# Kernel optimization log

Measured on AMD Instinct MI355X. Metric: run time of the kernel, lower is better.

## Reference

```python
import jax, jax.numpy as jnp
import numpy as np

B, S, U, H = 4, 2048, 1024, 8
HD = U // H
EPS = 1e-8


def setup_inputs() -> dict:
    key = jax.random.key(0)
    ks = jax.random.split(key, 10)
    sc = 1.0 / np.sqrt(U)
    x = jax.random.normal(ks[0], (B, S, U), dtype=jnp.float32)
    Wq = jax.random.normal(ks[1], (U, U), dtype=jnp.float32) * sc
    bq = jnp.zeros((U,), dtype=jnp.float32)
    Wk = jax.random.normal(ks[2], (U, U), dtype=jnp.float32) * sc
    bk = jnp.zeros((U,), dtype=jnp.float32)
    Wv = jax.random.normal(ks[3], (U, U), dtype=jnp.float32) * sc
    bv = jnp.zeros((U,), dtype=jnp.float32)
    Wr = jax.random.normal(ks[4], (U, U), dtype=jnp.float32) * sc
    br = jnp.zeros((U,), dtype=jnp.float32)
    gamma = jnp.ones((U,), dtype=jnp.float32)
    beta = jnp.zeros((U,), dtype=jnp.float32)
    return {"x": x, "Wq": Wq, "bq": bq, "Wk": Wk, "bk": bk, "Wv": Wv,
            "bv": bv, "Wr": Wr, "br": br, "gamma": gamma, "beta": beta}


def reference(x, Wq, bq, Wk, bk, Wv, bv, Wr, br, gamma, beta):
    relu = jax.nn.relu
    q = relu(jnp.einsum('bsu,uv->bsv', x, Wq) + bq)
    k = relu(jnp.einsum('bsu,uv->bsv', x, Wk) + bk)
    v = relu(jnp.einsum('bsu,uv->bsv', x, Wv) + bv)
    res = relu(jnp.einsum('bsu,uv->bsv', x, Wr) + br)
    # Faithful to the original: a raw reshape (NOT split+transpose head split).
    q = q.reshape(B * H, S, HD)
    k = k.reshape(B * H, S, HD)
    v = v.reshape(B * H, S, HD)
    scores = jnp.einsum('nqd,nkd->nqk', q, k) / jnp.sqrt(jnp.float32(HD))
    weights = jax.nn.softmax(scores, axis=-1)
    # dropout_rate = 0.0 -> identity
    attn = jnp.einsum('nqk,nkd->nqd', weights, v)
    attn = attn.reshape(B, S, U)
    out = relu(attn + res)
    # custom LayerNorm (biased variance, eps inside sqrt)
    mean = jnp.mean(out, axis=-1, keepdims=True)
    var = jnp.mean(jnp.square(out - mean), axis=-1, keepdims=True)
    normed = (out - mean) / jnp.sqrt(var + EPS)
    return gamma * normed + beta
```

## Files before the change

kernel.cpp:

```cpp
#include <hip/hip_runtime.h>

typedef _Float16 half8_t __attribute__((ext_vector_type(8)));
typedef _Float16 half4_t __attribute__((ext_vector_type(4)));
typedef float floatx4 __attribute__((ext_vector_type(4)));

#define S_LEN 2048
#define U_DIM 1024
#define HD 128
#define M_TOT 8192
#define NHEADS 32


__device__ __forceinline__ void stage16(void* lds_base, const void* g_lane, int lane) {
#if defined(__has_builtin) && __has_builtin(__builtin_amdgcn_global_load_lds)
    __builtin_amdgcn_global_load_lds(
        (const __attribute__((address_space(1))) unsigned int*)g_lane,
        (__attribute__((address_space(3))) unsigned int*)lds_base, 16, 0, 0);
#else
    *(float4*)((char*)lds_base + lane * 16) = *(const float4*)g_lane;
#endif
}

__device__ __forceinline__ int swz(int row) { return (row >> 1) & 3; }

__global__ __launch_bounds__(256) void k_convert_x(const float* __restrict__ x,
                                                   _Float16* __restrict__ xh) {
    size_t i = (size_t)blockIdx.x * 256 + threadIdx.x;
    float4 v = ((const float4*)x)[i];
    half4_t h;
    h[0] = (_Float16)v.x; h[1] = (_Float16)v.y;
    h[2] = (_Float16)v.z; h[3] = (_Float16)v.w;
    ((half4_t*)xh)[i] = h;
}

__global__ __launch_bounds__(256) void k_transpose_w(const float* __restrict__ Wq,
                                                     const float* __restrict__ Wk,
                                                     const float* __restrict__ Wv,
                                                     const float* __restrict__ Wr,
                                                     _Float16* __restrict__ wt) {
    const int z = blockIdx.z;
    const float* W = (z == 0) ? Wq : (z == 1) ? Wk : (z == 2) ? Wv : Wr;
    _Float16* o = wt + (size_t)z * U_DIM * U_DIM;
    __shared__ float t[64][65];
    const int n0 = blockIdx.x * 64, k0 = blockIdx.y * 64;
    const int tid = threadIdx.x;
    for (int c = tid; c < 1024; c += 256) {
        int kk = c >> 4, nn = (c & 15) * 4;
        float4 v = *(const float4*)&W[(size_t)(k0 + kk) * U_DIM + n0 + nn];
        t[kk][nn] = v.x; t[kk][nn + 1] = v.y; t[kk][nn + 2] = v.z; t[kk][nn + 3] = v.w;
    }
    __syncthreads();
    for (int c = tid; c < 512; c += 256) {
        int nn = c >> 3, ks = (c & 7) * 8;
        half8_t h;
        for (int i = 0; i < 8; i++) h[i] = (_Float16)t[ks + i][nn];
        *(half8_t*)&o[(size_t)(n0 + nn) * U_DIM + k0 + ks] = h;
    }
}

__global__ __launch_bounds__(256) void k_qkvr_gemm(const _Float16* __restrict__ xh,
                                                   const _Float16* __restrict__ wt,
                                                   const float* __restrict__ bq,
                                                   const float* __restrict__ bk,
                                                   const float* __restrict__ bv,
                                                   const float* __restrict__ br,
                                                   _Float16* __restrict__ qh,
                                                   _Float16* __restrict__ kh,
                                                   _Float16* __restrict__ vh,
                                                   _Float16* __restrict__ resh) {
    const int b = blockIdx.x;
    const int xcd = b & 7, s = b >> 3;
    const int pair = xcd + 8 * (s & 3);
    const int m0 = (s >> 2) * 128;
    const int n0 = (pair & 7) * 128;
    const int z = pair >> 3;
    const _Float16* wz = wt + (size_t)z * U_DIM * U_DIM;

    __shared__ __align__(16) char AsB[8192];
    __shared__ __align__(16) char BsB[8192];
    __shared__ __align__(16) _Float16 Cs[128][136];

    const int tid = threadIdx.x;
    const int wave = tid >> 6, lane = tid & 63;
    const int lrow = lane & 15, quad = lane >> 4;
    const int wm = (wave >> 1) * 64, wn = (wave & 1) * 64;
    const int lr4 = lane >> 2;
    const int sseg = ((lane & 3) ^ swz(lr4)) * 16;

    floatx4 acc[4][4];
    for (int i = 0; i < 4; i++)
        for (int j = 0; j < 4; j++) acc[i][j] = (floatx4)0.0f;

    const char* xb = (const char*)xh;
    const char* wb = (const char*)wz;
    const int rsw = (quad ^ swz(lrow)) * 16;

    for (int k0 = 0; k0 < U_DIM; k0 += 32) {
        for (int t = 0; t < 2; t++) {
            int c = wave * 2 + t;
            stage16(AsB + c * 1024,
                    xb + (size_t)(m0 + c * 16 + lr4) * 2048 + k0 * 2 + sseg, lane);
            stage16(BsB + c * 1024,
                    wb + (size_t)(n0 + c * 16 + lr4) * 2048 + k0 * 2 + sseg, lane);
        }
        __syncthreads();
        half8_t af[4], bf[4];
        for (int i = 0; i < 4; i++)
            af[i] = *(const half8_t*)(AsB + ((wave >> 1) * 4 + i) * 1024 + lrow * 64 + rsw);
        for (int j = 0; j < 4; j++)
            bf[j] = *(const half8_t*)(BsB + ((wave & 1) * 4 + j) * 1024 + lrow * 64 + rsw);
        for (int i = 0; i < 4; i++)
            for (int j = 0; j < 4; j++)
                acc[i][j] = __builtin_amdgcn_mfma_f32_16x16x32_f16(af[i], bf[j], acc[i][j], 0, 0, 0);
        __syncthreads();
    }

    const float* bias = (z == 0) ? bq : (z == 1) ? bk : (z == 2) ? bv : br;
    _Float16* dst = (z == 0) ? qh : (z == 1) ? kh : (z == 2) ? vh : resh;

    for (int i = 0; i < 4; i++) {
        for (int j = 0; j < 4; j++) {
            int col = wn + j * 16 + lrow;
            float bcol = bias[n0 + col];
            for (int r = 0; r < 4; r++) {
                float v = acc[i][j][r] + bcol;
                Cs[wm + i * 16 + quad * 4 + r][col] = (_Float16)(v > 0.f ? v : 0.f);
            }
        }
    }
    __syncthreads();
    for (int c = tid; c < 2048; c += 256) {
        int row = c >> 4, seg = (c & 15) * 8;
        *(half8_t*)&dst[(size_t)(m0 + row) * U_DIM + n0 + seg] = *(half8_t*)&Cs[row][seg];
    }
}

__global__ __launch_bounds__(256) void k_transpose_v(const _Float16* __restrict__ vh,
                                                     _Float16* __restrict__ vt) {
    const int n = blockIdx.z;
    const int s0 = blockIdx.x * 64, d0 = blockIdx.y * 64;
    const _Float16* V = vh + (size_t)n * S_LEN * HD;
    _Float16* O = vt + (size_t)n * HD * S_LEN;
    __shared__ _Float16 t[64][72];
    const int tid = threadIdx.x;
    for (int c = tid; c < 512; c += 256) {
        int srow = c >> 3, off = (c & 7) * 8;
        *(half8_t*)&t[srow][off] = *(const half8_t*)&V[(size_t)(s0 + srow) * HD + d0 + off];
    }
    __syncthreads();
    for (int c = tid; c < 512; c += 256) {
        int drow = c >> 3, soff = (c & 7) * 8;
        half8_t h;
        for (int i = 0; i < 8; i++) h[i] = t[soff + i][drow];
        *(half8_t*)&O[(size_t)(d0 + drow) * S_LEN + s0 + soff] = h;
    }
}

__global__ __launch_bounds__(256, 2) void k_flash(const _Float16* __restrict__ qh,
                                                  const _Float16* __restrict__ kh,
                                                  const _Float16* __restrict__ vt,
                                                  float* __restrict__ Opart,
                                                  float* __restrict__ lpart) {
    const int head = blockIdx.x + 8 * (blockIdx.y & 3);
    const int m0 = (int)(blockIdx.y >> 2) * 128;
    const int kv2 = blockIdx.z;
    const _Float16* Q = qh + (size_t)head * S_LEN * HD;
    const char* Kb = (const char*)(kh + (size_t)head * S_LEN * HD);
    const char* Vb = (const char*)(vt + (size_t)head * HD * S_LEN);

    __shared__ __align__(16) char smem[51200];
    _Float16* Ps = (_Float16*)(smem + 32768);

    const int tid = threadIdx.x;
    const int w = tid >> 6, lane = tid & 63;
    const int lrow = lane & 15, quad = lane >> 4;
    const int lr4 = lane >> 2;
    const int sseg = ((lane & 3) ^ swz(lr4)) * 16;
    const int rsw = (quad ^ swz(lrow)) * 16;

    half8_t qf[2][4];
    for (int i = 0; i < 2; i++)
        for (int k0 = 0; k0 < 4; k0++)
            qf[i][k0] = *(const half8_t*)&Q[(size_t)(m0 + w * 32 + i * 16 + lrow) * HD + k0 * 32 + quad * 8];

    floatx4 acc_o[2][8];
    for (int i = 0; i < 2; i++)
        for (int j = 0; j < 8; j++) acc_o[i][j] = (floatx4)0.0f;
    float lp[2] = {0.0f, 0.0f};

    const float C1 = 0.12751742f;
    const int kt_end = kv2 * 16 + 16;

    for (int kt = kv2 * 16; kt < kt_end; ++kt) {
        if (kt != kv2 * 16) __syncthreads();
        for (int t = 0; t < 4; t++) {
            int c = w * 4 + t;
            int k0 = c >> 2, j = c & 3;
            stage16(smem + c * 1024,
                    Kb + (size_t)(kt * 64 + j * 16 + lr4) * 256 + k0 * 64 + sseg, lane);
        }
        for (int t = 0; t < 4; t++) {
            int c = w * 4 + t;
            int k0s = c >> 3, dg = c & 7;
            stage16(smem + 16384 + c * 1024,
                    Vb + (size_t)(dg * 16 + lr4) * 4096 + kt * 128 + k0s * 64 + sseg, lane);
        }
        __syncthreads();

        floatx4 acc_t[2][4];
        for (int i = 0; i < 2; i++)
            for (int j = 0; j < 4; j++) acc_t[i][j] = (floatx4)0.0f;
        for (int k0 = 0; k0 < 4; k0++)
            for (int j = 0; j < 4; j++) {
                half8_t kf = *(const half8_t*)(smem + (k0 * 4 + j) * 1024 + lrow * 64 + rsw);
                for (int i = 0; i < 2; i++)
                    acc_t[i][j] = __builtin_amdgcn_mfma_f32_16x16x32_f16(kf, qf[i][k0], acc_t[i][j], 0, 0, 0);
            }

        for (int i = 0; i < 2; i++)
            for (int j = 0; j < 4; j++) {
                floatx4 sv = acc_t[i][j] * C1 - 6.0f;
                half4_t ph;
                float p0 = exp2f(sv[0]), p1 = exp2f(sv[1]);
                float p2 = exp2f(sv[2]), p3 = exp2f(sv[3]);
                ph[0] = (_Float16)p0; ph[1] = (_Float16)p1;
                ph[2] = (_Float16)p2; ph[3] = (_Float16)p3;
                lp[i] += (p0 + p1) + (p2 + p3);
                *(half4_t*)&Ps[(w * 32 + i * 16 + lrow) * 72 + j * 16 + quad * 4] = ph;
            }

        for (int k0s = 0; k0s < 2; k0s++) {
            half8_t af[2];
            for (int i = 0; i < 2; i++)
                af[i] = *(const half8_t*)&Ps[(w * 32 + i * 16 + lrow) * 72 + k0s * 32 + quad * 8];
            for (int j = 0; j < 8; j++) {
                half8_t bv = *(const half8_t*)(smem + 16384 + (k0s * 8 + j) * 1024 + lrow * 64 + rsw);
                for (int i = 0; i < 2; i++)
                    acc_o[i][j] = __builtin_amdgcn_mfma_f32_16x16x32_f16(af[i], bv, acc_o[i][j], 0, 0, 0);
            }
        }
    }

    for (int i = 0; i < 2; i++) {
        lp[i] += __shfl_xor(lp[i], 16, 64);
        lp[i] += __shfl_xor(lp[i], 32, 64);
    }

    float* Od = Opart + (size_t)kv2 * ((size_t)NHEADS * S_LEN * HD) +
                ((size_t)head * S_LEN + m0) * HD;
    for (int i = 0; i < 2; i++)
        for (int j = 0; j < 8; j++)
            for (int r = 0; r < 4; r++)
                Od[(size_t)(w * 32 + i * 16 + quad * 4 + r) * HD + j * 16 + lrow] = acc_o[i][j][r];
    float* Ld = lpart + (size_t)kv2 * (NHEADS * S_LEN) + head * S_LEN + m0;
    if (quad == 0) {
        Ld[w * 32 + lrow] = lp[0];
        Ld[w * 32 + 16 + lrow] = lp[1];
    }
}

__global__ __launch_bounds__(256) void k_ln(const float* __restrict__ Opart,
                                            const float* __restrict__ lpart,
                                            const _Float16* __restrict__ resh,
                                            const float* __restrict__ gamma,
                                            const float* __restrict__ beta,
                                            float* __restrict__ out) {
    const int row = blockIdx.x;
    const int tid = threadIdx.x;
    const size_t e = (size_t)row * U_DIM + tid * 4;
    const size_t OH = (size_t)M_TOT * U_DIM;
    const int lidx = row * 8 + (tid >> 5);

    float4 a4 = *(const float4*)&Opart[e];
    float4 b4 = *(const float4*)&Opart[OH + e];
    float l = lpart[lidx] + lpart[NHEADS * S_LEN + lidx];
    float inv = 1.0f / l;
    half4_t rv = ((const half4_t*)(resh))[e >> 2];
    float4 gv = ((const float4*)gamma)[tid];
    float4 bv = ((const float4*)beta)[tid];

    float o[4];
    o[0] = fmaxf((a4.x + b4.x) * inv + (float)rv[0], 0.f);
    o[1] = fmaxf((a4.y + b4.y) * inv + (float)rv[1], 0.f);
    o[2] = fmaxf((a4.z + b4.z) * inv + (float)rv[2], 0.f);
    o[3] = fmaxf((a4.w + b4.w) * inv + (float)rv[3], 0.f);

    float s1 = (o[0] + o[1]) + (o[2] + o[3]);
    float s2 = (o[0] * o[0] + o[1] * o[1]) + (o[2] * o[2] + o[3] * o[3]);
    for (int off = 32; off; off >>= 1) {
        s1 += __shfl_xor(s1, off, 64);
        s2 += __shfl_xor(s2, off, 64);
    }
    __shared__ float red[8];
    const int wv = tid >> 6;
    if ((tid & 63) == 0) { red[wv] = s1; red[4 + wv] = s2; }
    __syncthreads();
    float ts1 = red[0] + red[1] + red[2] + red[3];
    float ts2 = red[4] + red[5] + red[6] + red[7];
    float mean = ts1 * (1.0f / 1024.0f);
    float var = ts2 * (1.0f / 1024.0f) - mean * mean;
    float rstd = rsqrtf(var + 1e-8f);
    float4 ov;
    ov.x = gv.x * (o[0] - mean) * rstd + bv.x;
    ov.y = gv.y * (o[1] - mean) * rstd + bv.y;
    ov.z = gv.z * (o[2] - mean) * rstd + bv.z;
    ov.w = gv.w * (o[3] - mean) * rstd + bv.w;
    ((float4*)(out))[e >> 2] = ov;
}

extern "C" void kernel_launch(void* const* d_in, const int* in_sizes, int n_in,
                              void* d_out, int out_size, void* d_ws, size_t ws_size,
                              hipStream_t stream) {
    const float* x     = (const float*)d_in[0];
    const float* Wq    = (const float*)d_in[1];
    const float* bq    = (const float*)d_in[2];
    const float* Wk    = (const float*)d_in[3];
    const float* bk    = (const float*)d_in[4];
    const float* Wv    = (const float*)d_in[5];
    const float* bv    = (const float*)d_in[6];
    const float* Wr    = (const float*)d_in[7];
    const float* br    = (const float*)d_in[8];
    const float* gamma = (const float*)d_in[9];
    const float* beta  = (const float*)d_in[10];
    float* out = (float*)d_out;

    char* p = (char*)d_ws;
    _Float16* xh = (_Float16*)p;    p += (size_t)M_TOT * U_DIM * 2;
    _Float16* wt = (_Float16*)p;    p += (size_t)4 * U_DIM * U_DIM * 2;
    _Float16* qh = (_Float16*)p;    p += (size_t)M_TOT * U_DIM * 2;
    _Float16* kh = (_Float16*)p;    p += (size_t)M_TOT * U_DIM * 2;
    _Float16* vh = (_Float16*)p;    p += (size_t)M_TOT * U_DIM * 2;
    _Float16* vt = (_Float16*)p;    p += (size_t)M_TOT * U_DIM * 2;
    _Float16* resh = (_Float16*)p;  p += (size_t)M_TOT * U_DIM * 2;
    float* Opart = (float*)p;       p += (size_t)2 * M_TOT * U_DIM * 4;
    float* lpart = (float*)p;

    k_convert_x<<<8192, 256, 0, stream>>>(x, xh);
    k_transpose_w<<<dim3(16, 16, 4), 256, 0, stream>>>(Wq, Wk, Wv, Wr, wt);
    k_qkvr_gemm<<<2048, 256, 0, stream>>>(xh, wt, bq, bk, bv, br, qh, kh, vh, resh);
    k_transpose_v<<<dim3(32, 2, 32), 256, 0, stream>>>(vh, vt);
    k_flash<<<dim3(8, 64, 2), 256, 0, stream>>>(qh, kh, vt, Opart, lpart);
    k_ln<<<8192, 256, 0, stream>>>(Opart, lpart, resh, gamma, beta, out);
}
```

Baseline: 307.0 us.

## Prefetch next tiles into registers, replacing direct global-to-LDS loads

In both the projection GEMM and the attention kernel, the direct global_load_lds staging is replaced by register prefetching. The next K-tile is loaded into registers while the current tile is being computed, then written to LDS at the top of the next iteration. The __syncthreads barriers become a custom s_waitcnt lgkmcnt(0) plus s_barrier, so vector-memory prefetches are not waited on at each barrier. This aims to hide global load latency behind MFMA work, at the cost of more registers (possible occupancy loss) and an extra barrier per attention iteration.

```diff
diff --git a/kernel.cpp b/kernel.cpp
--- a/kernel.cpp
+++ b/kernel.cpp
@@ -11,14 +11,8 @@
 #define NHEADS 32
 
 
-__device__ __forceinline__ void stage16(void* lds_base, const void* g_lane, int lane) {
-#if defined(__has_builtin) && __has_builtin(__builtin_amdgcn_global_load_lds)
-    __builtin_amdgcn_global_load_lds(
-        (const __attribute__((address_space(1))) unsigned int*)g_lane,
-        (__attribute__((address_space(3))) unsigned int*)lds_base, 16, 0, 0);
-#else
-    *(float4*)((char*)lds_base + lane * 16) = *(const float4*)g_lane;
-#endif
+__device__ __forceinline__ void barrier_lgkm() {
+    __asm__ volatile("s_waitcnt lgkmcnt(0)\ns_barrier" ::: "memory");
 }
 
 __device__ __forceinline__ int swz(int row) { return (row >> 1) & 3; }
@@ -86,24 +80,33 @@
     const int wm = (wave >> 1) * 64, wn = (wave & 1) * 64;
     const int lr4 = lane >> 2;
     const int sseg = ((lane & 3) ^ swz(lr4)) * 16;
+    const int rsw = (quad ^ swz(lrow)) * 16;
 
     floatx4 acc[4][4];
     for (int i = 0; i < 4; i++)
         for (int j = 0; j < 4; j++) acc[i][j] = (floatx4)0.0f;
 
-    const char* xb = (const char*)xh;
-    const char* wb = (const char*)wz;
-    const int rsw = (quad ^ swz(lrow)) * 16;
+    const char* xsrc = (const char*)xh + (size_t)(m0 + wave * 32 + lr4) * 2048 + sseg;
+    const char* wsrc = (const char*)wz + (size_t)(n0 + wave * 32 + lr4) * 2048 + sseg;
+
+    float4 areg[2], breg[2];
+    for (int t = 0; t < 2; t++) {
+        areg[t] = *(const float4*)(xsrc + t * 16 * 2048);
+        breg[t] = *(const float4*)(wsrc + t * 16 * 2048);
+    }
 
     for (int k0 = 0; k0 < U_DIM; k0 += 32) {
         for (int t = 0; t < 2; t++) {
-            int c = wave * 2 + t;
-            stage16(AsB + c * 1024,
-                    xb + (size_t)(m0 + c * 16 + lr4) * 2048 + k0 * 2 + sseg, lane);
-            stage16(BsB + c * 1024,
-                    wb + (size_t)(n0 + c * 16 + lr4) * 2048 + k0 * 2 + sseg, lane);
-        }
-        __syncthreads();
+            *(float4*)(AsB + (wave * 2 + t) * 1024 + lane * 16) = areg[t];
+            *(float4*)(BsB + (wave * 2 + t) * 1024 + lane * 16) = breg[t];
+        }
+        barrier_lgkm();
+        if (k0 + 32 < U_DIM) {
+            for (int t = 0; t < 2; t++) {
+                areg[t] = *(const float4*)(xsrc + t * 16 * 2048 + (k0 + 32) * 2);
+                breg[t] = *(const float4*)(wsrc + t * 16 * 2048 + (k0 + 32) * 2);
+            }
+        }
         half8_t af[4], bf[4];
         for (int i = 0; i < 4; i++)
             af[i] = *(const half8_t*)(AsB + ((wave >> 1) * 4 + i) * 1024 + lrow * 64 + rsw);
@@ -112,7 +115,7 @@
         for (int i = 0; i < 4; i++)
             for (int j = 0; j < 4; j++)
                 acc[i][j] = __builtin_amdgcn_mfma_f32_16x16x32_f16(af[i], bf[j], acc[i][j], 0, 0, 0);
-        __syncthreads();
+        barrier_lgkm();
     }
 
     const float* bias = (z == 0) ? bq : (z == 1) ? bk : (z == 2) ? bv : br;
@@ -189,23 +192,34 @@
     float lp[2] = {0.0f, 0.0f};
 
     const float C1 = 0.12751742f;
-    const int kt_end = kv2 * 16 + 16;
-
-    for (int kt = kv2 * 16; kt < kt_end; ++kt) {
-        if (kt != kv2 * 16) __syncthreads();
+    const int kt0 = kv2 * 16, kt_end = kt0 + 16;
+
+    const char* ksrc[4];
+    const char* vsrc[4];
+    for (int t = 0; t < 4; t++) {
+        int c = w * 4 + t;
+        ksrc[t] = Kb + (size_t)((c & 3) * 16 + lr4) * 256 + (c >> 2) * 64 + sseg;
+        vsrc[t] = Vb + (size_t)((c & 7) * 16 + lr4) * 4096 + (c >> 3) * 64 + sseg;
+    }
+
+    float4 kreg[4], vreg[4];
+    for (int t = 0; t < 4; t++) {
+        kreg[t] = *(const float4*)(ksrc[t] + (size_t)kt0 * 16384);
+        vreg[t] = *(const float4*)(vsrc[t] + kt0 * 128);
+    }
+
+    for (int kt = kt0; kt < kt_end; ++kt) {
         for (int t = 0; t < 4; t++) {
-            int c = w * 4 + t;
-            int k0 = c >> 2, j = c & 3;
-            stage16(smem + c * 1024,
-                    Kb + (size_t)(kt * 64 + j * 16 + lr4) * 256 + k0 * 64 + sseg, lane);
-        }
-        for (int t = 0; t < 4; t++) {
-            int c = w * 4 + t;
-            int k0s = c >> 3, dg = c & 7;
-            stage16(smem + 16384 + c * 1024,
-                    Vb + (size_t)(dg * 16 + lr4) * 4096 + kt * 128 + k0s * 64 + sseg, lane);
-        }
-        __syncthreads();
+            *(float4*)(smem + (w * 4 + t) * 1024 + lane * 16) = kreg[t];
+            *(float4*)(smem + 16384 + (w * 4 + t) * 1024 + lane * 16) = vreg[t];
+        }
+        barrier_lgkm();
+        if (kt + 1 < kt_end) {
+            for (int t = 0; t < 4; t++) {
+                kreg[t] = *(const float4*)(ksrc[t] + (size_t)(kt + 1) * 16384);
+                vreg[t] = *(const float4*)(vsrc[t] + (kt + 1) * 128);
+            }
+        }
 
         floatx4 acc_t[2][4];
         for (int i = 0; i < 2; i++)
@@ -239,6 +253,7 @@
                     acc_o[i][j] = __builtin_amdgcn_mfma_f32_16x16x32_f16(af[i], bv, acc_o[i][j], 0, 0, 0);
             }
         }
+        barrier_lgkm();
     }
 
     for (int i = 0; i < 2; i++) {
```

New measurement: 619.9 us. +101.9%, slower.
